# Optimization experiments

Hardware: AMD Instinct MI355X
Metric: run time of the kernel (lower is better)

## Reference

```python
import jax, jax.numpy as jnp
import numpy as np

N = 50000
IN_CH = 128
HID = 32
HEADS = 3
OUT_CH = 128
E = 800000
NEG_SLOPE = 0.2
BN_EPS = 1e-5


def _glorot(key, shape):
    fan = shape[0] + shape[-1]
    s = jnp.sqrt(6.0 / fan)
    return jax.random.uniform(key, shape, jnp.float32, -s, s)


def setup_inputs() -> dict:
    key = jax.random.key(0)
    ks = jax.random.split(key, 12)
    x = jax.random.normal(ks[0], (N, IN_CH), jnp.float32)
    edge_index = jax.random.randint(ks[1], (2, E), 0, N, jnp.int64)
    # GATConv 1: in -> HID per head, HEADS heads, concat
    W1 = _glorot(ks[2], (IN_CH, HEADS * HID))
    att_src1 = _glorot(ks[3], (HEADS, HID))
    att_dst1 = _glorot(ks[4], (HEADS, HID))
    b1 = jnp.zeros((HEADS * HID,), jnp.float32)
    # GATConv 2: HEADS*HID -> OUT_CH, 1 head
    W2 = _glorot(ks[5], (HEADS * HID, OUT_CH))
    att_src2 = _glorot(ks[6], (1, OUT_CH))
    att_dst2 = _glorot(ks[7], (1, OUT_CH))
    b2 = jnp.zeros((OUT_CH,), jnp.float32)
    # BatchNorm params
    bn_gamma = jnp.ones((OUT_CH,), jnp.float32)
    bn_beta = jnp.zeros((OUT_CH,), jnp.float32)
    # residual Linear
    Wres = _glorot(ks[8], (IN_CH, OUT_CH))
    bres = jnp.zeros((OUT_CH,), jnp.float32)
    return dict(x=x, edge_index=edge_index, W1=W1, att_src1=att_src1,
                att_dst1=att_dst1, b1=b1, W2=W2, att_src2=att_src2,
                att_dst2=att_dst2, b2=b2, bn_gamma=bn_gamma, bn_beta=bn_beta,
                Wres=Wres, bres=bres)


def gat_conv(x, W, a_src, a_dst, b, src, dst, n, heads, ch):
    """PyG GATConv (eval mode, self-loops already in src/dst)."""
    h = (x @ W).reshape(n, heads, ch)                    # [N,H,C]
    a_s = jnp.sum(h * a_src[None], axis=-1)              # [N,H]
    a_d = jnp.sum(h * a_dst[None], axis=-1)              # [N,H]
    e = a_s[src] + a_d[dst]                              # [E,H]
    e = jnp.where(e > 0, e, NEG_SLOPE * e)               # leaky_relu
    m = jax.ops.segment_max(e, dst, num_segments=n)      # softmax over edges into dst
    e = jnp.exp(e - m[dst])
    denom = jax.ops.segment_sum(e, dst, num_segments=n)
    alpha = e / (denom[dst] + 1e-16)                     # [E,H]
    out = jax.ops.segment_sum(h[src] * alpha[:, :, None], dst, num_segments=n)
    return out.reshape(n, heads * ch) + b


def reference(x, edge_index, W1, att_src1, att_dst1, b1, W2, att_src2,
              att_dst2, b2, bn_gamma, bn_beta, Wres, bres):
    n = x.shape[0]
    loop = jnp.arange(n, dtype=edge_index.dtype)
    src = jnp.concatenate([edge_index[0], loop])         # add self-loops (PyG default)
    dst = jnp.concatenate([edge_index[1], loop])
    residual = x @ Wres + bres
    out = gat_conv(x, W1, att_src1, att_dst1, b1, src, dst, n, HEADS, HID)
    out = gat_conv(out, W2, att_src2, att_dst2, b2, src, dst, n, 1, OUT_CH)
    # BatchNorm1d, training-mode batch statistics
    mu = jnp.mean(out, axis=0)
    var = jnp.var(out, axis=0)
    out = (out - mu) * jax.lax.rsqrt(var + BN_EPS) * bn_gamma + bn_beta
    out = jax.nn.relu(out)
    return out + residual
```

## Files before the change

kernel.cpp:

```cpp
#include <hip/hip_runtime.h>

#define NEG 0.2f
#define NEG_INF (-1e30f)

typedef __attribute__((ext_vector_type(8))) short bf16x8;
typedef __attribute__((ext_vector_type(4))) float f32x4;

__device__ __forceinline__ float leaky(float e) { return e > 0.f ? e : NEG * e; }

__device__ __forceinline__ unsigned short f2bf(float f) {
    unsigned int u = __float_as_uint(f);
    unsigned int r = u + 0x7fffu + ((u >> 16) & 1u);
    return (unsigned short)(r >> 16);
}
__device__ __forceinline__ float2 bf2f2(unsigned int u) {
    float2 r;
    r.x = __uint_as_float(u << 16);
    r.y = __uint_as_float(u & 0xffff0000u);
    return r;
}

__device__ __forceinline__ void pack_w(const float* __restrict__ W,
                                       unsigned short* __restrict__ Bp, int K, int N, int idx) {
    int i = idx & 7;
    int rest = idx >> 3;
    int lane = rest & 63;
    rest >>= 6;
    int KT = K / 32;
    int kt = rest % KT;
    int ct = rest / KT;
    int m = lane & 15, kb = lane >> 4;
    int k = kt * 32 + kb * 8 + i, col = ct * 16 + m;
    Bp[idx] = f2bf(W[(size_t)k * N + col]);
}

__global__ __launch_bounds__(256) void prep_kernel(const float* __restrict__ x,
                                                   unsigned short* __restrict__ xb, int n4,
                                                   const float* __restrict__ W1,
                                                   unsigned short* __restrict__ w1p,
                                                   const float* __restrict__ W2,
                                                   unsigned short* __restrict__ w2p,
                                                   const float* __restrict__ Wres,
                                                   unsigned short* __restrict__ wresp,
                                                   const int* __restrict__ dst, int E,
                                                   int* __restrict__ bucketCnt, int nbk,
                                                   int binBlks) {
    int b = blockIdx.x;
    if (b < binBlks) {
        __shared__ int hist[1600];
        for (int k = threadIdx.x; k < nbk; k += 256) hist[k] = 0;
        __syncthreads();
        int c0 = b * 4096;
        int cnt = min(4096, E - c0);
        for (int i = threadIdx.x; i < cnt; i += 256)
            atomicAdd(&hist[dst[c0 + i] >> 5], 1);
        __syncthreads();
        for (int k = threadIdx.x; k < nbk; k += 256) {
            int h = hist[k];
            if (h) atomicAdd(&bucketCnt[k], h);
        }
        return;
    }
    b -= binBlks;
    int nxb = (n4 + 255) / 256;
    if (b < nxb) {
        int i = b * 256 + threadIdx.x;
        if (i < n4) {
            float4 v = ((const float4*)x)[i];
            ushort4 o;
            o.x = f2bf(v.x); o.y = f2bf(v.y); o.z = f2bf(v.z); o.w = f2bf(v.w);
            ((ushort4*)xb)[i] = o;
        }
        return;
    }
    b -= nxb;
    if (b < 48) { pack_w(W1, w1p, 128, 96, b * 256 + threadIdx.x); return; }
    b -= 48;
    if (b < 48) { pack_w(W2, w2p, 96, 128, b * 256 + threadIdx.x); return; }
    b -= 48;
    if (b < 64) { pack_w(Wres, wresp, 128, 128, b * 256 + threadIdx.x); }
}

__global__ __launch_bounds__(1024) void scan_buckets(const int* __restrict__ bc,
                                                     int* __restrict__ pairBase,
                                                     int* __restrict__ bcur,
                                                     int* __restrict__ offs, int nbk, int n) {
    __shared__ int buf[1024];
    __shared__ int carry;
    int tid = threadIdx.x;
    if (tid == 0) carry = 0;
    __syncthreads();
    for (int base = 0; base < nbk; base += 1024) {
        int v = (base + tid < nbk) ? bc[base + tid] : 0;
        buf[tid] = v;
        __syncthreads();
        for (int s = 1; s < 1024; s <<= 1) {
            int t = (tid >= s) ? buf[tid - s] : 0;
            __syncthreads();
            buf[tid] += t;
            __syncthreads();
        }
        int incl = buf[tid];
        int tot = buf[1023];
        int c = carry;
        if (base + tid < nbk) {
            int ex = c + incl - v;
            pairBase[base + tid] = ex;
            bcur[base + tid] = ex;
        }
        __syncthreads();
        if (tid == 0) carry = c + tot;
        __syncthreads();
    }
    if (tid == 0) {
        pairBase[nbk] = carry;
        offs[n] = carry;
    }
}

__global__ __launch_bounds__(256) void bin_kernel(const int* __restrict__ src,
                                                  const int* __restrict__ dst, int E,
                                                  int* __restrict__ bcur,
                                                  int2* __restrict__ pairBuf, int nb) {
    __shared__ int2 stage[4096];
    __shared__ int hist[1600];
    __shared__ int base[1600];
    for (int c0 = blockIdx.x * 4096; c0 < E; c0 += gridDim.x * 4096) {
        int cnt = min(4096, E - c0);
        for (int b = threadIdx.x; b < nb; b += 256) hist[b] = 0;
        __syncthreads();
        for (int i = threadIdx.x; i < cnt; i += 256) {
            int s = src[c0 + i], d = dst[c0 + i];
            stage[i] = make_int2(s, d);
            atomicAdd(&hist[d >> 5], 1);
        }
        __syncthreads();
        for (int b = threadIdx.x; b < nb; b += 256) {
            int h = hist[b];
            if (h) base[b] = atomicAdd(&bcur[b], h);
            hist[b] = 0;
        }
        __syncthreads();
        for (int i = threadIdx.x; i < cnt; i += 256) {
            int2 p = stage[i];
            int b = p.y >> 5;
            int off = atomicAdd(&hist[b], 1);
            pairBuf[base[b] + off] = p;
        }
        __syncthreads();
    }
}

template <int K, int N, int HEADS>
__device__ __forceinline__ void gemm_body(int w, const unsigned short* __restrict__ A,
                                          const unsigned short* __restrict__ Bp,
                                          const float* __restrict__ bias,
                                          unsigned short* __restrict__ outB,
                                          const float* __restrict__ asrc,
                                          const float* __restrict__ adst,
                                          float* __restrict__ a_s,
                                          float* __restrict__ a_d, int M) {
    constexpr int KT = K / 32, CT = N / 16;
    int row0 = w * 16;
    if (row0 >= M) return;
    int lane = threadIdx.x & 63;
    int m = lane & 15, kb = lane >> 4;
    const unsigned short* arow = A + (size_t)(row0 + m) * K + kb * 8;

    f32x4 acc[CT];
#pragma unroll
    for (int ct = 0; ct < CT; ++ct) acc[ct] = (f32x4){0.f, 0.f, 0.f, 0.f};

#pragma unroll
    for (int kt = 0; kt < KT; ++kt) {
        bf16x8 a = *(const bf16x8*)(arow + kt * 32);
#pragma unroll
        for (int ct = 0; ct < CT; ++ct) {
            bf16x8 b = *(const bf16x8*)(Bp + ((size_t)(ct * KT + kt) * 64 + lane) * 8);
            acc[ct] = __builtin_amdgcn_mfma_f32_16x16x32_bf16(a, b, acc[ct], 0, 0, 0);
        }
    }

#pragma unroll
    for (int r = 0; r < 4; ++r) {
        int row = row0 + kb * 4 + r;
#pragma unroll
        for (int ct = 0; ct < CT; ++ct) {
            int col = ct * 16 + m;
            float v = acc[ct][r] + (bias ? bias[col] : 0.f);
            outB[(size_t)row * N + col] = f2bf(v);
        }
    }

    if (HEADS > 0) {
        float asv[CT], adv[CT];
#pragma unroll
        for (int ct = 0; ct < CT; ++ct) {
            int col = ct * 16 + m;
            asv[ct] = asrc[col];
            adv[ct] = adst[col];
        }
        constexpr int TPH = CT / (HEADS > 0 ? HEADS : 1);
#pragma unroll
        for (int r = 0; r < 4; ++r) {
            int row = row0 + kb * 4 + r;
#pragma unroll
            for (int h = 0; h < HEADS; ++h) {
                float s = 0.f, d = 0.f;
#pragma unroll
                for (int t = 0; t < TPH; ++t) {
                    int ct = h * TPH + t;
                    s += acc[ct][r] * asv[ct];
                    d += acc[ct][r] * adv[ct];
                }
#pragma unroll
                for (int off = 1; off <= 8; off <<= 1) {
                    s += __shfl_xor(s, off);
                    d += __shfl_xor(d, off);
                }
                if (m == 0) {
                    a_s[(size_t)row * HEADS + h] = s;
                    a_d[(size_t)row * HEADS + h] = d;
                }
            }
        }
    }
}

__global__ __launch_bounds__(256) void phase2_kernel(
    const int2* __restrict__ pairBuf, const int* __restrict__ pairBase,
    const int* __restrict__ bcur, int* __restrict__ offs,
    int* __restrict__ csr, int nb,
    const unsigned short* __restrict__ xb,
    const unsigned short* __restrict__ w1p, unsigned short* __restrict__ h1b,
    const float* __restrict__ asrc1, const float* __restrict__ adst1,
    float* __restrict__ as1, float* __restrict__ ad1,
    const unsigned short* __restrict__ wresp, const float* __restrict__ bres,
    unsigned short* __restrict__ residb, int n, int passBlks, int g1Blks) {
    int b = blockIdx.x;
    int lane = threadIdx.x & 63;
    int wid = threadIdx.x >> 6;
    if (b < passBlks) {
        __shared__ int cnt[4][32];
        int bk = b * 4 + wid;
        if (bk < nb) {
            int node0 = bk * 32;
            int lo = pairBase[bk], hi = bcur[bk];
            if (lane < 32) cnt[wid][lane] = 0;
            for (int i = lo + lane; i < hi; i += 64)
                atomicAdd(&cnt[wid][pairBuf[i].y & 31], 1);
            int myc = (lane < 32) ? cnt[wid][lane] : 0;
            int c = myc;
#pragma unroll
            for (int s = 1; s < 32; s <<= 1) {
                int t = __shfl_up(c, s);
                if (lane >= s && lane < 32) c += t;
            }
            int basePos = lo + c - myc;
            if (lane < 32) {
                if (node0 + lane < n) offs[node0 + lane] = basePos;
                cnt[wid][lane] = basePos;
            }
            for (int i = lo + lane; i < hi; i += 64) {
                int2 p = pairBuf[i];
                int pos = atomicAdd(&cnt[wid][p.y & 31], 1);
                csr[pos] = p.x;
            }
        }
        return;
    }
    b -= passBlks;
    if (b < g1Blks) {
        gemm_body<128, 96, 3>(b * 4 + wid, xb, w1p, nullptr, h1b,
                              asrc1, adst1, as1, ad1, n);
        return;
    }
    b -= g1Blks;
    gemm_body<128, 128, 0>(b * 4 + wid, xb, wresp, bres, residb,
                           nullptr, nullptr, nullptr, nullptr, n);
}

__global__ __launch_bounds__(256) void gemm2_kernel(const unsigned short* __restrict__ A,
                                                    const unsigned short* __restrict__ Bp,
                                                    unsigned short* __restrict__ outB,
                                                    const float* __restrict__ asrc,
                                                    const float* __restrict__ adst,
                                                    float* __restrict__ a_s,
                                                    float* __restrict__ a_d, int M) {
    gemm_body<96, 128, 1>(blockIdx.x * 4 + (threadIdx.x >> 6), A, Bp, nullptr, outB,
                          asrc, adst, a_s, a_d, M);
}

__global__ __launch_bounds__(256) void gat1_agg(const unsigned short* __restrict__ h1b,
                                                const float* __restrict__ a_s,
                                                const float* __restrict__ a_d,
                                                const int* __restrict__ offs,
                                                const int* __restrict__ csr,
                                                const float* __restrict__ b1,
                                                unsigned short* __restrict__ out1b, int n) {
    __shared__ int ssrc[4][64];
    __shared__ float se[4][3][64];
    int wid = threadIdx.x >> 6;
    int node = blockIdx.x * 4 + wid;
    if (node >= n) return;
    int lane = threadIdx.x & 63;
    int head = lane >> 4; if (head > 2) head = 2;
    int beg = offs[node], end = offs[node + 1];
    int deg = end - beg;
    float ad0 = a_d[node * 3 + 0], ad1 = a_d[node * 3 + 1], ad2 = a_d[node * 3 + 2];
    float es0 = leaky(a_s[node * 3 + 0] + ad0);
    float es1 = leaky(a_s[node * 3 + 1] + ad1);
    float es2 = leaky(a_s[node * 3 + 2] + ad2);
    float2 hv0 = make_float2(0.f, 0.f);
    if (lane < 48) hv0 = bf2f2(*(const unsigned int*)&h1b[(size_t)node * 96 + 2 * lane]);

    float den;
    float2 acc;

    if (deg <= 64) {
        int s = 0;
        float l0 = NEG_INF, l1 = NEG_INF, l2 = NEG_INF;
        if (lane < deg) {
            s = csr[beg + lane];
            l0 = leaky(a_s[s * 3 + 0] + ad0);
            l1 = leaky(a_s[s * 3 + 1] + ad1);
            l2 = leaky(a_s[s * 3 + 2] + ad2);
        }
        float m0 = l0, m1 = l1, m2 = l2;
#pragma unroll
        for (int sh = 32; sh >= 1; sh >>= 1) {
            m0 = fmaxf(m0, __shfl_xor(m0, sh));
            m1 = fmaxf(m1, __shfl_xor(m1, sh));
            m2 = fmaxf(m2, __shfl_xor(m2, sh));
        }
        m0 = fmaxf(m0, es0); m1 = fmaxf(m1, es1); m2 = fmaxf(m2, es2);
        float e0 = 0.f, e1 = 0.f, e2 = 0.f;
        if (lane < deg) {
            e0 = __expf(l0 - m0); e1 = __expf(l1 - m1); e2 = __expf(l2 - m2);
        }
        ssrc[wid][lane] = s;
        se[wid][0][lane] = e0; se[wid][1][lane] = e1; se[wid][2][lane] = e2;
        float w0 = __expf(es0 - m0), w1 = __expf(es1 - m1), w2 = __expf(es2 - m2);
        den = (head == 0) ? w0 : ((head == 1) ? w1 : w2);
        float wSelf = (lane < 16) ? w0 : ((lane < 32) ? w1 : w2);
        acc.x = wSelf * hv0.x; acc.y = wSelf * hv0.y;

        int jj = 0;
        for (; jj + 7 < deg; jj += 8) {
            int sA[8]; float wA[8]; unsigned ph[8];
#pragma unroll
            for (int q = 0; q < 8; ++q) {
                sA[q] = ssrc[wid][jj + q];
                wA[q] = se[wid][head][jj + q];
            }
#pragma unroll
            for (int q = 0; q < 8; ++q)
                ph[q] = (lane < 48) ? *(const unsigned*)&h1b[(size_t)sA[q] * 96 + 2 * lane] : 0u;
            float dsum = 0.f;
#pragma unroll
            for (int q = 0; q < 8; ++q) {
                dsum += wA[q];
                if (lane < 48) {
                    float2 h = bf2f2(ph[q]);
                    acc.x += wA[q] * h.x; acc.y += wA[q] * h.y;
                }
            }
            den += dsum;
        }
        for (; jj + 3 < deg; jj += 4) {
            int sA[4]; float wA[4]; unsigned ph[4];
#pragma unroll
            for (int q = 0; q < 4; ++q) {
                sA[q] = ssrc[wid][jj + q];
                wA[q] = se[wid][head][jj + q];
            }
#pragma unroll
            for (int q = 0; q < 4; ++q)
                ph[q] = (lane < 48) ? *(const unsigned*)&h1b[(size_t)sA[q] * 96 + 2 * lane] : 0u;
            float dsum = 0.f;
#pragma unroll
            for (int q = 0; q < 4; ++q) {
                dsum += wA[q];
                if (lane < 48) {
                    float2 h = bf2f2(ph[q]);
                    acc.x += wA[q] * h.x; acc.y += wA[q] * h.y;
                }
            }
            den += dsum;
        }
        for (; jj < deg; ++jj) {
            int sA = ssrc[wid][jj];
            float wA = se[wid][head][jj];
            den += wA;
            if (lane < 48) {
                float2 ha = bf2f2(*(const unsigned*)&h1b[(size_t)sA * 96 + 2 * lane]);
                acc.x += wA * ha.x; acc.y += wA * ha.y;
            }
        }
    } else {
        float m0 = es0, m1 = es1, m2 = es2;
        for (int j = beg + lane; j < end; j += 64) {
            int s = csr[j];
            m0 = fmaxf(m0, leaky(a_s[s * 3 + 0] + ad0));
            m1 = fmaxf(m1, leaky(a_s[s * 3 + 1] + ad1));
            m2 = fmaxf(m2, leaky(a_s[s * 3 + 2] + ad2));
        }
#pragma unroll
        for (int sh = 32; sh >= 1; sh >>= 1) {
            m0 = fmaxf(m0, __shfl_xor(m0, sh));
            m1 = fmaxf(m1, __shfl_xor(m1, sh));
            m2 = fmaxf(m2, __shfl_xor(m2, sh));
        }
        float w0 = __expf(es0 - m0), w1 = __expf(es1 - m1), w2 = __expf(es2 - m2);
        den = (head == 0) ? w0 : ((head == 1) ? w1 : w2);
        float wSelf = (lane < 16) ? w0 : ((lane < 32) ? w1 : w2);
        acc.x = wSelf * hv0.x; acc.y = wSelf * hv0.y;
        for (int t0 = beg; t0 < end; t0 += 64) {
            int cnt = min(64, end - t0);
            int s = 0;
            float e0 = 0.f, e1 = 0.f, e2 = 0.f;
            if (lane < cnt) {
                s = csr[t0 + lane];
                e0 = __expf(leaky(a_s[s * 3 + 0] + ad0) - m0);
                e1 = __expf(leaky(a_s[s * 3 + 1] + ad1) - m1);
                e2 = __expf(leaky(a_s[s * 3 + 2] + ad2) - m2);
            }
            ssrc[wid][lane] = s;
            se[wid][0][lane] = e0; se[wid][1][lane] = e1; se[wid][2][lane] = e2;
            int jj = 0;
            for (; jj + 7 < cnt; jj += 8) {
                int sA[8]; float wA[8]; unsigned ph[8];
#pragma unroll
                for (int q = 0; q < 8; ++q) {
                    sA[q] = ssrc[wid][jj + q];
                    wA[q] = se[wid][head][jj + q];
                }
#pragma unroll
                for (int q = 0; q < 8; ++q)
                    ph[q] = (lane < 48) ? *(const unsigned*)&h1b[(size_t)sA[q] * 96 + 2 * lane] : 0u;
                float dsum = 0.f;
#pragma unroll
                for (int q = 0; q < 8; ++q) {
                    dsum += wA[q];
                    if (lane < 48) {
                        float2 h = bf2f2(ph[q]);
                        acc.x += wA[q] * h.x; acc.y += wA[q] * h.y;
                    }
                }
                den += dsum;
            }
            for (; jj < cnt; ++jj) {
                int sA = ssrc[wid][jj];
                float wA = se[wid][head][jj];
                den += wA;
                if (lane < 48) {
                    float2 ha = bf2f2(*(const unsigned*)&h1b[(size_t)sA * 96 + 2 * lane]);
                    acc.x += wA * ha.x; acc.y += wA * ha.y;
                }
            }
        }
    }

    if (lane < 48) {
        float inv = 1.f / (den + 1e-16f);
        ushort2 o;
        o.x = f2bf(acc.x * inv + b1[2 * lane]);
        o.y = f2bf(acc.y * inv + b1[2 * lane + 1]);
        *(ushort2*)&out1b[(size_t)node * 96 + 2 * lane] = o;
    }
}

__global__ __launch_bounds__(256) void gat2_agg(const unsigned short* __restrict__ h2b,
                                                const float* __restrict__ a_s,
                                                const float* __restrict__ a_d,
                                                const int* __restrict__ offs,
                                                const int* __restrict__ csr,
                                                const float* __restrict__ b2,
                                                unsigned short* __restrict__ out2b,
                                                float* __restrict__ part, int n) {
    __shared__ int ssrc[4][64];
    __shared__ float se[4][64];
    __shared__ float4 red[4][64];
    int wid = threadIdx.x >> 6;
    int node = blockIdx.x * 4 + wid;
    int lane = threadIdx.x & 63;
    float2 o = make_float2(0.f, 0.f);

    if (node < n) {
        int beg = offs[node], end = offs[node + 1];
        int deg = end - beg;
        float ad = a_d[node];
        float es = leaky(a_s[node] + ad);
        float2 hv0 = bf2f2(*(const unsigned int*)&h2b[(size_t)node * 128 + 2 * lane]);
        float den;
        float2 acc;

        if (deg <= 64) {
            int s = 0;
            float l = NEG_INF;
            if (lane < deg) {
                s = csr[beg + lane];
                l = leaky(a_s[s] + ad);
            }
            float m = l;
#pragma unroll
            for (int sh = 32; sh >= 1; sh >>= 1) m = fmaxf(m, __shfl_xor(m, sh));
            m = fmaxf(m, es);
            float e = (lane < deg) ? __expf(l - m) : 0.f;
            ssrc[wid][lane] = s;
            se[wid][lane] = e;
            float wSelf = __expf(es - m);
            den = wSelf;
            acc.x = wSelf * hv0.x; acc.y = wSelf * hv0.y;

            int jj = 0;
            for (; jj + 7 < deg; jj += 8) {
                int sA[8]; float wA[8]; unsigned ph[8];
#pragma unroll
                for (int q = 0; q < 8; ++q) {
                    sA[q] = ssrc[wid][jj + q];
                    wA[q] = se[wid][jj + q];
                }
#pragma unroll
                for (int q = 0; q < 8; ++q)
                    ph[q] = *(const unsigned*)&h2b[(size_t)sA[q] * 128 + 2 * lane];
                float dsum = 0.f;
#pragma unroll
                for (int q = 0; q < 8; ++q) {
                    dsum += wA[q];
                    float2 h = bf2f2(ph[q]);
                    acc.x += wA[q] * h.x; acc.y += wA[q] * h.y;
                }
                den += dsum;
            }
            for (; jj + 3 < deg; jj += 4) {
                int sA[4]; float wA[4]; unsigned ph[4];
#pragma unroll
                for (int q = 0; q < 4; ++q) {
                    sA[q] = ssrc[wid][jj + q];
                    wA[q] = se[wid][jj + q];
                }
#pragma unroll
                for (int q = 0; q < 4; ++q)
                    ph[q] = *(const unsigned*)&h2b[(size_t)sA[q] * 128 + 2 * lane];
                float dsum = 0.f;
#pragma unroll
                for (int q = 0; q < 4; ++q) {
                    dsum += wA[q];
                    float2 h = bf2f2(ph[q]);
                    acc.x += wA[q] * h.x; acc.y += wA[q] * h.y;
                }
                den += dsum;
            }
            for (; jj < deg; ++jj) {
                int sA = ssrc[wid][jj];
                float wA = se[wid][jj];
                den += wA;
                float2 ha = bf2f2(*(const unsigned*)&h2b[(size_t)sA * 128 + 2 * lane]);
                acc.x += wA * ha.x; acc.y += wA * ha.y;
            }
        } else {
            float m = es;
            for (int j = beg + lane; j < end; j += 64) {
                int s = csr[j];
                m = fmaxf(m, leaky(a_s[s] + ad));
            }
#pragma unroll
            for (int sh = 32; sh >= 1; sh >>= 1) m = fmaxf(m, __shfl_xor(m, sh));
            float wSelf = __expf(es - m);
            den = wSelf;
            acc.x = wSelf * hv0.x; acc.y = wSelf * hv0.y;
            for (int t0 = beg; t0 < end; t0 += 64) {
                int cnt = min(64, end - t0);
                int s = 0;
                float e = 0.f;
                if (lane < cnt) {
                    s = csr[t0 + lane];
                    e = __expf(leaky(a_s[s] + ad) - m);
                }
                ssrc[wid][lane] = s;
                se[wid][lane] = e;
                int jj = 0;
                for (; jj + 7 < cnt; jj += 8) {
                    int sA[8]; float wA[8]; unsigned ph[8];
#pragma unroll
                    for (int q = 0; q < 8; ++q) {
                        sA[q] = ssrc[wid][jj + q];
                        wA[q] = se[wid][jj + q];
                    }
#pragma unroll
                    for (int q = 0; q < 8; ++q)
                        ph[q] = *(const unsigned*)&h2b[(size_t)sA[q] * 128 + 2 * lane];
                    float dsum = 0.f;
#pragma unroll
                    for (int q = 0; q < 8; ++q) {
                        dsum += wA[q];
                        float2 h = bf2f2(ph[q]);
                        acc.x += wA[q] * h.x; acc.y += wA[q] * h.y;
                    }
                    den += dsum;
                }
                for (; jj < cnt; ++jj) {
                    int sA = ssrc[wid][jj];
                    float wA = se[wid][jj];
                    den += wA;
                    float2 ha = bf2f2(*(const unsigned*)&h2b[(size_t)sA * 128 + 2 * lane]);
                    acc.x += wA * ha.x; acc.y += wA * ha.y;
                }
            }
        }

        float inv = 1.f / (den + 1e-16f);
        o.x = acc.x * inv + b2[2 * lane];
        o.y = acc.y * inv + b2[2 * lane + 1];
        ushort2 ob;
        ob.x = f2bf(o.x); ob.y = f2bf(o.y);
        *(ushort2*)&out2b[(size_t)node * 128 + 2 * lane] = ob;
    }

    red[wid][lane] = make_float4(o.x, o.y, o.x * o.x, o.y * o.y);
    __syncthreads();
    if (wid == 0) {
        float4 a = red[0][lane], b = red[1][lane], c = red[2][lane], d = red[3][lane];
        float sx = a.x + b.x + c.x + d.x;
        float sy = a.y + b.y + c.y + d.y;
        float qx = a.z + b.z + c.z + d.z;
        float qy = a.w + b.w + c.w + d.w;
        float* p = part + (size_t)(blockIdx.x & 63) * 256;
        atomicAdd(&p[2 * lane + 0], sx);
        atomicAdd(&p[2 * lane + 1], sy);
        atomicAdd(&p[128 + 2 * lane + 0], qx);
        atomicAdd(&p[128 + 2 * lane + 1], qy);
    }
}

__global__ void bn_finalize(const float* __restrict__ part, const float* __restrict__ gamma,
                            const float* __restrict__ beta, float* __restrict__ ss, int n) {
    int c = threadIdx.x;
    float S = 0.f, Q = 0.f;
    for (int k = 0; k < 64; ++k) {
        S += part[(size_t)k * 256 + c];
        Q += part[(size_t)k * 256 + 128 + c];
    }
    float invN = 1.f / (float)n;
    float mu = S * invN;
    float var = Q * invN - mu * mu;
    float g = gamma[c] * rsqrtf(var + 1e-5f);
    ss[c] = g;
    ss[128 + c] = beta[c] - mu * g;
}

__global__ void final_kernel(const unsigned short* __restrict__ out2b,
                             const unsigned short* __restrict__ residb,
                             const float* __restrict__ ss, float* __restrict__ out, int n) {
    int i = blockIdx.x * blockDim.x + threadIdx.x;
    if (i >= n * 32) return;
    int c0 = (i & 31) * 4;
    uint2 v = ((const uint2*)out2b)[i];
    uint2 r = ((const uint2*)residb)[i];
    float2 v01 = bf2f2(v.x), v23 = bf2f2(v.y);
    float2 r01 = bf2f2(r.x), r23 = bf2f2(r.y);
    float4 o;
    o.x = fmaxf(v01.x * ss[c0 + 0] + ss[128 + c0 + 0], 0.f) + r01.x;
    o.y = fmaxf(v01.y * ss[c0 + 1] + ss[128 + c0 + 1], 0.f) + r01.y;
    o.z = fmaxf(v23.x * ss[c0 + 2] + ss[128 + c0 + 2], 0.f) + r23.x;
    o.w = fmaxf(v23.y * ss[c0 + 3] + ss[128 + c0 + 3], 0.f) + r23.y;
    ((float4*)out)[i] = o;
}

extern "C" void kernel_launch(void* const* d_in, const int* in_sizes, int n_in,
                              void* d_out, int out_size, void* d_ws, size_t ws_size,
                              hipStream_t stream) {
    const float* x     = (const float*)d_in[0];
    const int*   ei    = (const int*)d_in[1];
    const float* W1    = (const float*)d_in[2];
    const float* asrc1 = (const float*)d_in[3];
    const float* adst1 = (const float*)d_in[4];
    const float* b1    = (const float*)d_in[5];
    const float* W2    = (const float*)d_in[6];
    const float* asrc2 = (const float*)d_in[7];
    const float* adst2 = (const float*)d_in[8];
    const float* b2    = (const float*)d_in[9];
    const float* gamma = (const float*)d_in[10];
    const float* beta  = (const float*)d_in[11];
    const float* Wres  = (const float*)d_in[12];
    const float* bres  = (const float*)d_in[13];

    const int n = in_sizes[0] / 128;
    const int E = in_sizes[1] / 2;

    char* ws = (char*)d_ws;
    size_t off = 0;
    auto alloc = [&](size_t bytes) {
        void* p = ws + off;
        off = (off + bytes + 255) & ~(size_t)255;
        return p;
    };
    float* as1  = (float*)alloc((size_t)n * 3 * 4);
    float* ad1  = (float*)alloc((size_t)n * 3 * 4);
    float* as2  = (float*)alloc((size_t)n * 4);
    float* ad2  = (float*)alloc((size_t)n * 4);
    float* part = (float*)alloc(64 * 256 * 4);
    float* ss   = (float*)alloc(256 * 4);
    unsigned short* xb     = (unsigned short*)alloc((size_t)n * 128 * 2);
    unsigned short* h1b    = (unsigned short*)alloc((size_t)n * 96 * 2);
    unsigned short* h2b    = (unsigned short*)alloc((size_t)n * 128 * 2);
    unsigned short* out1b  = (unsigned short*)alloc((size_t)n * 96 * 2);
    unsigned short* out2b  = (unsigned short*)alloc((size_t)n * 128 * 2);
    unsigned short* residb = (unsigned short*)alloc((size_t)n * 128 * 2);
    unsigned short* w1p    = (unsigned short*)alloc(128 * 96 * 2);
    unsigned short* w2p    = (unsigned short*)alloc(96 * 128 * 2);
    unsigned short* wresp  = (unsigned short*)alloc(128 * 128 * 2);
    int* offs      = (int*)alloc((size_t)(n + 1) * 4);
    int* bucketCnt = (int*)alloc(1600 * 4);
    int* pairBase  = (int*)alloc(1601 * 4);
    int* bcur      = (int*)alloc(1600 * 4);
    int2* pairBuf  = (int2*)alloc((size_t)E * 8);
    int* csr       = (int*)alloc((size_t)E * 4);

    hipMemsetAsync(bucketCnt, 0, 1600 * 4, stream);
    hipMemsetAsync(part, 0, 64 * 256 * 4, stream);

    const int* srcIdx = ei;
    const int* dstIdx = ei + E;
    const int NB = (n + 31) / 32;
    const int binBlks = (E + 4095) / 4096;

    const int nxb = (n * 32 + 255) / 256;
    prep_kernel<<<binBlks + nxb + 160, 256, 0, stream>>>(x, xb, n * 32, W1, w1p, W2, w2p,
                                                         Wres, wresp, dstIdx, E,
                                                         bucketCnt, NB, binBlks);

    scan_buckets<<<1, 1024, 0, stream>>>(bucketCnt, pairBase, bcur, offs, NB, n);

    bin_kernel<<<binBlks, 256, 0, stream>>>(srcIdx, dstIdx, E, bcur, pairBuf, NB);

    const int mt = (n + 15) / 16;
    const int gblk = (mt + 3) / 4;
    const int passBlks = 391;

    phase2_kernel<<<passBlks + 2 * gblk, 256, 0, stream>>>(
        pairBuf, pairBase, bcur, offs, csr, NB, xb, w1p, h1b, asrc1, adst1, as1, ad1,
        wresp, bres, residb, n, passBlks, gblk);

    gat1_agg<<<(n + 3) / 4, 256, 0, stream>>>(h1b, as1, ad1, offs, csr, b1, out1b, n);
    gemm2_kernel<<<gblk, 256, 0, stream>>>(out1b, w2p, h2b, asrc2, adst2, as2, ad2, n);
    gat2_agg<<<(n + 3) / 4, 256, 0, stream>>>(h2b, as2, ad2, offs, csr, b2, out2b, part, n);
    bn_finalize<<<1, 128, 0, stream>>>(part, gamma, beta, ss, n);
    final_kernel<<<(n * 32 + 255) / 256, 256, 0, stream>>>(out2b, residb, ss, (float*)d_out, n);
}
```

Measured before the change: 164.9 us.

## Split GAT1 aggregation across two waves per node; co-schedule residual GEMM

```diff
diff --git a/kernel.cpp b/kernel.cpp
--- a/kernel.cpp
+++ b/kernel.cpp
@@ -84,10 +84,12 @@
 __global__ __launch_bounds__(1024) void scan_buckets(const int* __restrict__ bc,
                                                      int* __restrict__ pairBase,
                                                      int* __restrict__ bcur,
-                                                     int* __restrict__ offs, int nbk, int n) {
+                                                     int* __restrict__ offs, int nbk, int n,
+                                                     float* __restrict__ part) {
     __shared__ int buf[1024];
     __shared__ int carry;
     int tid = threadIdx.x;
+    for (int i = tid; i < 64 * 256; i += 1024) part[i] = 0.f;
     if (tid == 0) carry = 0;
     __syncthreads();
     for (int base = 0; base < nbk; base += 1024) {
@@ -234,9 +236,7 @@
     const unsigned short* __restrict__ xb,
     const unsigned short* __restrict__ w1p, unsigned short* __restrict__ h1b,
     const float* __restrict__ asrc1, const float* __restrict__ adst1,
-    float* __restrict__ as1, float* __restrict__ ad1,
-    const unsigned short* __restrict__ wresp, const float* __restrict__ bres,
-    unsigned short* __restrict__ residb, int n, int passBlks, int g1Blks) {
+    float* __restrict__ as1, float* __restrict__ ad1, int n, int passBlks) {
     int b = blockIdx.x;
     int lane = threadIdx.x & 63;
     int wid = threadIdx.x >> 6;
@@ -270,14 +270,7 @@
         return;
     }
     b -= passBlks;
-    if (b < g1Blks) {
-        gemm_body<128, 96, 3>(b * 4 + wid, xb, w1p, nullptr, h1b,
-                              asrc1, adst1, as1, ad1, n);
-        return;
-    }
-    b -= g1Blks;
-    gemm_body<128, 128, 0>(b * 4 + wid, xb, wresp, bres, residb,
-                           nullptr, nullptr, nullptr, nullptr, n);
+    gemm_body<128, 96, 3>(b * 4 + wid, xb, w1p, nullptr, h1b, asrc1, adst1, as1, ad1, n);
 }
 
 __global__ __launch_bounds__(256) void gemm2_kernel(const unsigned short* __restrict__ A,
@@ -291,62 +284,91 @@
                           asrc, adst, a_s, a_d, M);
 }
 
-__global__ __launch_bounds__(256) void gat1_agg(const unsigned short* __restrict__ h1b,
-                                                const float* __restrict__ a_s,
-                                                const float* __restrict__ a_d,
-                                                const int* __restrict__ offs,
-                                                const int* __restrict__ csr,
-                                                const float* __restrict__ b1,
-                                                unsigned short* __restrict__ out1b, int n) {
+__global__ __launch_bounds__(256) void gat1_res_kernel(
+    const unsigned short* __restrict__ h1b,
+    const float* __restrict__ a_s, const float* __restrict__ a_d,
+    const int* __restrict__ offs, const int* __restrict__ csr,
+    const float* __restrict__ b1, unsigned short* __restrict__ out1b,
+    const unsigned short* __restrict__ xb, const unsigned short* __restrict__ wresp,
+    const float* __restrict__ bres, unsigned short* __restrict__ residb,
+    int n, int gresBlks) {
+    int b = blockIdx.x;
+    int wid = threadIdx.x >> 6, lane = threadIdx.x & 63;
+    if (b < gresBlks) {
+        gemm_body<128, 128, 0>(b * 4 + wid, xb, wresp, bres, residb,
+                               nullptr, nullptr, nullptr, nullptr, n);
+        return;
+    }
+    b -= gresBlks;
     __shared__ int ssrc[4][64];
     __shared__ float se[4][3][64];
-    int wid = threadIdx.x >> 6;
-    int node = blockIdx.x * 4 + wid;
-    if (node >= n) return;
-    int lane = threadIdx.x & 63;
+    __shared__ float pm[4][3];
+    __shared__ float pden[4][3];
+    __shared__ float2 pacc[2][48];
+    int slot = wid >> 1, sub = wid & 1;
+    int node = b * 2 + slot;
+    bool valid = node < n;
+    int beg = 0, end = 0;
+    if (valid) { beg = offs[node]; end = offs[node + 1]; }
+    int deg = end - beg;
+    int half1 = (deg + 1) >> 1;
+    int myBeg = beg + (sub ? half1 : 0);
+    int myEnd = sub ? end : beg + half1;
+    float ad0 = 0.f, ad1 = 0.f, ad2 = 0.f, es0 = 0.f, es1 = 0.f, es2 = 0.f;
+    if (valid) {
+        ad0 = a_d[node * 3 + 0]; ad1 = a_d[node * 3 + 1]; ad2 = a_d[node * 3 + 2];
+        es0 = leaky(a_s[node * 3 + 0] + ad0);
+        es1 = leaky(a_s[node * 3 + 1] + ad1);
+        es2 = leaky(a_s[node * 3 + 2] + ad2);
+    }
     int head = lane >> 4; if (head > 2) head = 2;
-    int beg = offs[node], end = offs[node + 1];
-    int deg = end - beg;
-    float ad0 = a_d[node * 3 + 0], ad1 = a_d[node * 3 + 1], ad2 = a_d[node * 3 + 2];
-    float es0 = leaky(a_s[node * 3 + 0] + ad0);
-    float es1 = leaky(a_s[node * 3 + 1] + ad1);
-    float es2 = leaky(a_s[node * 3 + 2] + ad2);
-    float2 hv0 = make_float2(0.f, 0.f);
-    if (lane < 48) hv0 = bf2f2(*(const unsigned int*)&h1b[(size_t)node * 96 + 2 * lane]);
-
-    float den;
-    float2 acc;
-
-    if (deg <= 64) {
+
+    float m0 = NEG_INF, m1 = NEG_INF, m2 = NEG_INF;
+    for (int j = myBeg + lane; j < myEnd; j += 64) {
+        int s = csr[j];
+        m0 = fmaxf(m0, leaky(a_s[s * 3 + 0] + ad0));
+        m1 = fmaxf(m1, leaky(a_s[s * 3 + 1] + ad1));
+        m2 = fmaxf(m2, leaky(a_s[s * 3 + 2] + ad2));
+    }
+#pragma unroll
+    for (int sh = 32; sh >= 1; sh >>= 1) {
+        m0 = fmaxf(m0, __shfl_xor(m0, sh));
+        m1 = fmaxf(m1, __shfl_xor(m1, sh));
+        m2 = fmaxf(m2, __shfl_xor(m2, sh));
+    }
+    if (lane == 0) { pm[wid][0] = m0; pm[wid][1] = m1; pm[wid][2] = m2; }
+    __syncthreads();
+    {
+        int wA = slot * 2, wB = slot * 2 + 1;
+        m0 = fmaxf(fmaxf(pm[wA][0], pm[wB][0]), es0);
+        m1 = fmaxf(fmaxf(pm[wA][1], pm[wB][1]), es1);
+        m2 = fmaxf(fmaxf(pm[wA][2], pm[wB][2]), es2);
+    }
+
+    float den0 = 0.f, den1 = 0.f, den2 = 0.f;
+    float2 acc = make_float2(0.f, 0.f);
+    for (int t0 = myBeg; t0 < myEnd; t0 += 64) {
+        int cnt = min(64, myEnd - t0);
         int s = 0;
-        float l0 = NEG_INF, l1 = NEG_INF, l2 = NEG_INF;
-        if (lane < deg) {
-            s = csr[beg + lane];
-            l0 = leaky(a_s[s * 3 + 0] + ad0);
-            l1 = leaky(a_s[s * 3 + 1] + ad1);
-            l2 = leaky(a_s[s * 3 + 2] + ad2);
-        }
-        float m0 = l0, m1 = l1, m2 = l2;
-#pragma unroll
-        for (int sh = 32; sh >= 1; sh >>= 1) {
-            m0 = fmaxf(m0, __shfl_xor(m0, sh));
-            m1 = fmaxf(m1, __shfl_xor(m1, sh));
-            m2 = fmaxf(m2, __shfl_xor(m2, sh));
-        }
-        m0 = fmaxf(m0, es0); m1 = fmaxf(m1, es1); m2 = fmaxf(m2, es2);
         float e0 = 0.f, e1 = 0.f, e2 = 0.f;
-        if (lane < deg) {
-            e0 = __expf(l0 - m0); e1 = __expf(l1 - m1); e2 = __expf(l2 - m2);
+        if (lane < cnt) {
+            s = csr[t0 + lane];
+            e0 = __expf(leaky(a_s[s * 3 + 0] + ad0) - m0);
+            e1 = __expf(leaky(a_s[s * 3 + 1] + ad1) - m1);
+            e2 = __expf(leaky(a_s[s * 3 + 2] + ad2) - m2);
         }
         ssrc[wid][lane] = s;
         se[wid][0][lane] = e0; se[wid][1][lane] = e1; se[wid][2][lane] = e2;
-        float w0 = __expf(es0 - m0), w1 = __expf(es1 - m1), w2 = __expf(es2 - m2);
-        den = (head == 0) ? w0 : ((head == 1) ? w1 : w2);
-        float wSelf = (lane < 16) ? w0 : ((lane < 32) ? w1 : w2);
-        acc.x = wSelf * hv0.x; acc.y = wSelf * hv0.y;
-
+        float d0 = e0, d1 = e1, d2 = e2;
+#pragma unroll
+        for (int sh = 32; sh >= 1; sh >>= 1) {
+            d0 += __shfl_xor(d0, sh);
+            d1 += __shfl_xor(d1, sh);
+            d2 += __shfl_xor(d2, sh);
+        }
+        den0 += d0; den1 += d1; den2 += d2;
         int jj = 0;
-        for (; jj + 7 < deg; jj += 8) {
+        for (; jj + 7 < cnt; jj += 8) {
             int sA[8]; float wA[8]; unsigned ph[8];
 #pragma unroll
             for (int q = 0; q < 8; ++q) {
@@ -356,18 +378,15 @@
 #pragma unroll
             for (int q = 0; q < 8; ++q)
                 ph[q] = (lane < 48) ? *(const unsigned*)&h1b[(size_t)sA[q] * 96 + 2 * lane] : 0u;
-            float dsum = 0.f;
 #pragma unroll
             for (int q = 0; q < 8; ++q) {
-                dsum += wA[q];
                 if (lane < 48) {
                     float2 h = bf2f2(ph[q]);
                     acc.x += wA[q] * h.x; acc.y += wA[q] * h.y;
                 }
             }
-            den += dsum;
-        }
-        for (; jj + 3 < deg; jj += 4) {
+        }
+        for (; jj + 3 < cnt; jj += 4) {
             int sA[4]; float wA[4]; unsigned ph[4];
 #pragma unroll
             for (int q = 0; q < 4; ++q) {
@@ -377,91 +396,43 @@
 #pragma unroll
             for (int q = 0; q < 4; ++q)
                 ph[q] = (lane < 48) ? *(const unsigned*)&h1b[(size_t)sA[q] * 96 + 2 * lane] : 0u;
-            float dsum = 0.f;
 #pragma unroll
             for (int q = 0; q < 4; ++q) {
-                dsum += wA[q];
                 if (lane < 48) {
                     float2 h = bf2f2(ph[q]);
                     acc.x += wA[q] * h.x; acc.y += wA[q] * h.y;
                 }
             }
-            den += dsum;
-        }
-        for (; jj < deg; ++jj) {
+        }
+        for (; jj < cnt; ++jj) {
             int sA = ssrc[wid][jj];
-            float wA = se[wid][head][jj];
-            den += wA;
+            float wAq = se[wid][head][jj];
             if (lane < 48) {
                 float2 ha = bf2f2(*(const unsigned*)&h1b[(size_t)sA * 96 + 2 * lane]);
-                acc.x += wA * ha.x; acc.y += wA * ha.y;
-            }
-        }
-    } else {
-        float m0 = es0, m1 = es1, m2 = es2;
-        for (int j = beg + lane; j < end; j += 64) {
-            int s = csr[j];
-            m0 = fmaxf(m0, leaky(a_s[s * 3 + 0] + ad0));
-            m1 = fmaxf(m1, leaky(a_s[s * 3 + 1] + ad1));
-            m2 = fmaxf(m2, leaky(a_s[s * 3 + 2] + ad2));
-        }
-#pragma unroll
-        for (int sh = 32; sh >= 1; sh >>= 1) {
-            m0 = fmaxf(m0, __shfl_xor(m0, sh));
-            m1 = fmaxf(m1, __shfl_xor(m1, sh));
-            m2 = fmaxf(m2, __shfl_xor(m2, sh));
-        }
+                acc.x += wAq * ha.x; acc.y += wAq * ha.y;
+            }
+        }
+    }
+
+    if (sub == 0 && valid) {
         float w0 = __expf(es0 - m0), w1 = __expf(es1 - m1), w2 = __expf(es2 - m2);
-        den = (head == 0) ? w0 : ((head == 1) ? w1 : w2);
-        float wSelf = (lane < 16) ? w0 : ((lane < 32) ? w1 : w2);
-        acc.x = wSelf * hv0.x; acc.y = wSelf * hv0.y;
-        for (int t0 = beg; t0 < end; t0 += 64) {
-            int cnt = min(64, end - t0);
-            int s = 0;
-            float e0 = 0.f, e1 = 0.f, e2 = 0.f;
-            if (lane < cnt) {
-                s = csr[t0 + lane];
-                e0 = __expf(leaky(a_s[s * 3 + 0] + ad0) - m0);
-                e1 = __expf(leaky(a_s[s * 3 + 1] + ad1) - m1);
-                e2 = __expf(leaky(a_s[s * 3 + 2] + ad2) - m2);
-            }
-            ssrc[wid][lane] = s;
-            se[wid][0][lane] = e0; se[wid][1][lane] = e1; se[wid][2][lane] = e2;
-            int jj = 0;
-            for (; jj + 7 < cnt; jj += 8) {
-                int sA[8]; float wA[8]; unsigned ph[8];
-#pragma unroll
-                for (int q = 0; q < 8; ++q) {
-                    sA[q] = ssrc[wid][jj + q];
-                    wA[q] = se[wid][head][jj + q];
-                }
-#pragma unroll
-                for (int q = 0; q < 8; ++q)
-                    ph[q] = (lane < 48) ? *(const unsigned*)&h1b[(size_t)sA[q] * 96 + 2 * lane] : 0u;
-                float dsum = 0.f;
-#pragma unroll
-                for (int q = 0; q < 8; ++q) {
-                    dsum += wA[q];
-                    if (lane < 48) {
-                        float2 h = bf2f2(ph[q]);
-                        acc.x += wA[q] * h.x; acc.y += wA[q] * h.y;
-                    }
-                }
-                den += dsum;
-            }
-            for (; jj < cnt; ++jj) {
-                int sA = ssrc[wid][jj];
-                float wA = se[wid][head][jj];
-                den += wA;
-                if (lane < 48) {
-                    float2 ha = bf2f2(*(const unsigned*)&h1b[(size_t)sA * 96 + 2 * lane]);
-                    acc.x += wA * ha.x; acc.y += wA * ha.y;
-                }
-            }
-        }
-    }
-
-    if (lane < 48) {
+        den0 += w0; den1 += w1; den2 += w2;
+        if (lane < 48) {
+            float2 hv0 = bf2f2(*(const unsigned*)&h1b[(size_t)node * 96 + 2 * lane]);
+            float wS = (lane < 16) ? w0 : ((lane < 32) ? w1 : w2);
+            acc.x += wS * hv0.x; acc.y += wS * hv0.y;
+        }
+    }
+    if (lane == 0) { pden[wid][0] = den0; pden[wid][1] = den1; pden[wid][2] = den2; }
+    if (sub == 1 && lane < 48) pacc[slot][lane] = acc;
+    __syncthreads();
+    if (sub == 0 && valid && lane < 48) {
+        int wB = slot * 2 + 1;
+        float2 pa = pacc[slot][lane];
+        acc.x += pa.x; acc.y += pa.y;
+        float den = (lane < 16) ? den0 + pden[wB][0]
+                  : (lane < 32) ? den1 + pden[wB][1]
+                                : den2 + pden[wB][2];
         float inv = 1.f / (den + 1e-16f);
         ushort2 o;
         o.x = f2bf(acc.x * inv + b1[2 * lane]);
@@ -719,7 +690,6 @@
     int* csr       = (int*)alloc((size_t)E * 4);
 
     hipMemsetAsync(bucketCnt, 0, 1600 * 4, stream);
-    hipMemsetAsync(part, 0, 64 * 256 * 4, stream);
 
     const int* srcIdx = ei;
     const int* dstIdx = ei + E;
@@ -731,7 +701,7 @@
                                                          Wres, wresp, dstIdx, E,
                                                          bucketCnt, NB, binBlks);
 
-    scan_buckets<<<1, 1024, 0, stream>>>(bucketCnt, pairBase, bcur, offs, NB, n);
+    scan_buckets<<<1, 1024, 0, stream>>>(bucketCnt, pairBase, bcur, offs, NB, n, part);
 
     bin_kernel<<<binBlks, 256, 0, stream>>>(srcIdx, dstIdx, E, bcur, pairBuf, NB);
 
@@ -739,11 +709,14 @@
     const int gblk = (mt + 3) / 4;
     const int passBlks = 391;
 
-    phase2_kernel<<<passBlks + 2 * gblk, 256, 0, stream>>>(
+    phase2_kernel<<<passBlks + gblk, 256, 0, stream>>>(
         pairBuf, pairBase, bcur, offs, csr, NB, xb, w1p, h1b, asrc1, adst1, as1, ad1,
-        wresp, bres, residb, n, passBlks, gblk);
-
-    gat1_agg<<<(n + 3) / 4, 256, 0, stream>>>(h1b, as1, ad1, offs, csr, b1, out1b, n);
+        n, passBlks);
+
+    const int g1Blks = (n + 1) / 2;
+    gat1_res_kernel<<<gblk + g1Blks, 256, 0, stream>>>(
+        h1b, as1, ad1, offs, csr, b1, out1b, xb, wresp, bres, residb, n, gblk);
+
     gemm2_kernel<<<gblk, 256, 0, stream>>>(out1b, w2p, h2b, asrc2, adst2, as2, ad2, n);
     gat2_agg<<<(n + 3) / 4, 256, 0, stream>>>(h2b, as2, ad2, offs, csr, b2, out2b, part, n);
     bn_finalize<<<1, 128, 0, stream>>>(part, gamma, beta, ss, n);
```

New measurement: 249.7 us. +51.4%, slower.
